# Optimization experiments

Measured on AMD Instinct MI355X. Metric: run time of the kernel, lower is better.

Reference implementation:

```python
import jax, jax.numpy as jnp
import numpy as np

K = 3          # per-row / per-col topk, from init kwarg k
THRESHOLD = 0.0


def setup_inputs() -> dict:
    key = jax.random.key(0)
    k1, k2 = jax.random.split(key)
    P, R, S = 512, 256, 256
    matching_score_map = jax.random.normal(k1, (P, R, S), dtype=jnp.float32)
    node_corr_scores = jax.random.uniform(k2, (P,), dtype=jnp.float32)
    ref_knn_masks = jnp.ones((P, R), dtype=bool)
    src_knn_masks = jnp.ones((P, S), dtype=bool)
    return {
        "matching_score_map": matching_score_map,
        "node_corr_scores": node_corr_scores,
        "ref_knn_masks": ref_knn_masks,
        "src_knn_masks": src_knn_masks,
    }


def reference(matching_score_map, node_corr_scores, ref_knn_masks, src_knn_masks):
    # score map: exp of log-matching scores  [P, R, S]
    score = jnp.exp(matching_score_map)
    P, R, S = score.shape
    # valid correspondence mask  [P, R, S]
    corr_mask = ref_knn_masks[:, :, None] & src_knn_masks[:, None, :]

    p_idx = jnp.arange(P)[:, None, None]

    # topk along src axis (dim=2), scatter back into a zero map
    ref_vals, ref_idx = jax.lax.top_k(score, K)                      # [P, R, K]
    ref_score_map = jnp.zeros_like(score).at[
        p_idx, jnp.arange(R)[None, :, None], ref_idx
    ].set(ref_vals)

    # topk along ref axis (dim=1): transpose so it is the last axis
    src_vals, src_idx = jax.lax.top_k(score.transpose(0, 2, 1), K)   # [P, S, K]
    src_score_map = jnp.zeros_like(score).at[
        p_idx, src_idx, jnp.arange(S)[None, :, None]
    ].set(src_vals)

    ref_corr_map = (ref_score_map > THRESHOLD) & corr_mask
    src_corr_map = (src_score_map > THRESHOLD) & corr_mask

    score_map = (ref_score_map + src_score_map) * 0.5
    # mutual=False -> logical_or; conditional=False -> no node_corr_scores scaling
    corr_map = ref_corr_map | src_corr_map
    return score_map, corr_map
```

## Files before the change

kernel.cpp:

```cpp
#include <hip/hip_runtime.h>
#include <math.h>
#include <stdint.h>

#define Pn 512
#define Rn 256
#define Sn 256

typedef unsigned long long u64;
typedef unsigned int u32;

__device__ __forceinline__ u32 mono(float f) {
  u32 u = __float_as_uint(f);
  return (u & 0x80000000u) ? ~u : (u | 0x80000000u);
}
__device__ __forceinline__ float unmono(u32 m) {
  u32 bits = (m & 0x80000000u) ? (m & 0x7FFFFFFFu) : ~m;
  return __uint_as_float(bits);
}
__device__ __forceinline__ u64 makekey(float v, int idx) {
  return ((u64)mono(v) << 32) | (u32)(~(u32)idx);
}
__device__ __forceinline__ int key_idx(u64 k) { return (int)(~(u32)k); }
__device__ __forceinline__ float key_val(u64 k) { return unmono((u32)(k >> 32)); }

__device__ __forceinline__ void cswap(u64& a, u64& b) {
  const bool c = a > b;
  const u64 hi = c ? a : b;
  const u64 lo = c ? b : a;
  a = hi; b = lo;
}

#define COL_BLOCKS Pn
#define ROW_BLOCKS ((Pn * Rn) / 4)

__global__ __launch_bounds__(256) void top3_kernel(
    const float* __restrict__ score,
    float* __restrict__ refv, int* __restrict__ refi,
    float* __restrict__ srcv, int* __restrict__ srci) {
  if (blockIdx.x < COL_BLOCKS) {
    const int p = blockIdx.x;
    const int s = threadIdx.x;
    const float* base = score + (size_t)p * Rn * Sn + s;
    u64 t0 = 0, t1 = 0, t2 = 0;
    #pragma unroll 8
    for (int r = 0; r < Rn; ++r) {
      u64 k = makekey(base[(size_t)r * Sn], r);
      cswap(t0, k); cswap(t1, k); cswap(t2, k);
    }
    const size_t PS = (size_t)Pn * Sn;
    const size_t o  = (size_t)p * Sn + s;
    srcv[0 * PS + o] = expf(key_val(t0)); srci[0 * PS + o] = key_idx(t0);
    srcv[1 * PS + o] = expf(key_val(t1)); srci[1 * PS + o] = key_idx(t1);
    srcv[2 * PS + o] = expf(key_val(t2)); srci[2 * PS + o] = key_idx(t2);
  } else {
    const int bid  = blockIdx.x - COL_BLOCKS;
    const int row  = (bid * blockDim.x + threadIdx.x) >> 6;
    const int lane = threadIdx.x & 63;
    const float4 v = reinterpret_cast<const float4*>(score + (size_t)row * Sn)[lane];
    const int b = lane * 4;
    u64 a0 = makekey(v.x, b + 0);
    u64 a1 = makekey(v.y, b + 1);
    u64 a2 = makekey(v.z, b + 2);
    u64 a3 = makekey(v.w, b + 3);
    cswap(a0, a1); cswap(a2, a3); cswap(a0, a2); cswap(a1, a3); cswap(a1, a2);
    u64 t0 = a0, t1 = a1, t2 = a2;

    u64 res0 = 0, res1 = 0, res2 = 0;
    #pragma unroll
    for (int j = 0; j < 3; ++j) {
      u64 m = t0;
      #pragma unroll
      for (int off = 1; off < 64; off <<= 1) {
        const u64 o = __shfl_xor(m, off);
        m = (o > m) ? o : m;
      }
      const bool hit = (t0 == m);
      t0 = hit ? t1 : t0;
      t1 = hit ? t2 : t1;
      t2 = hit ? 0ull : t2;
      if (j == 0) res0 = m; else if (j == 1) res1 = m; else res2 = m;
    }
    if (lane == 0) {
      const size_t o = (size_t)row * 3;
      refv[o + 0] = expf(key_val(res0)); refi[o + 0] = key_idx(res0);
      refv[o + 1] = expf(key_val(res1)); refi[o + 1] = key_idx(res1);
      refv[o + 2] = expf(key_val(res2)); refi[o + 2] = key_idx(res2);
    }
  }
}

__device__ __forceinline__ void compute_elem(
    int s, int r, bool rmask, int sm,
    float rv0, float rv1, float rv2, int ri0, int ri1, int ri2,
    float a0, int b0, float a1, int b1, float a2, int b2,
    float& oscore, float& ocorr) {
  const float rv = (s == ri0) ? rv0 : (s == ri1) ? rv1 : (s == ri2) ? rv2 : 0.0f;
  const float sv = (r == b0) ? a0 : (r == b1) ? a1 : (r == b2) ? a2 : 0.0f;
  oscore = 0.5f * (rv + sv);
  const bool m = rmask && (sm != 0);
  ocorr = (((rv > 0.0f) || (sv > 0.0f)) && m) ? 1.0f : 0.0f;
}

__global__ __launch_bounds__(256) void write_kernel(
    const float* __restrict__ refv, const int* __restrict__ refi,
    const float* __restrict__ srcv, const int* __restrict__ srci,
    const int* __restrict__ rmaskp, const int* __restrict__ smaskp,
    float* __restrict__ out) {
  const int p     = blockIdx.x >> 2;
  const int rbase = (blockIdx.x & 3) * 64;
  const int warp  = threadIdx.x >> 6;
  const int lane  = threadIdx.x & 63;
  const size_t PS = (size_t)Pn * Sn;
  const size_t N  = (size_t)Pn * Rn * Sn;

  const float4 sv0 = reinterpret_cast<const float4*>(srcv + 0 * PS + (size_t)p * Sn)[lane];
  const float4 sv1 = reinterpret_cast<const float4*>(srcv + 1 * PS + (size_t)p * Sn)[lane];
  const float4 sv2 = reinterpret_cast<const float4*>(srcv + 2 * PS + (size_t)p * Sn)[lane];
  const int4   si0 = reinterpret_cast<const int4*>(srci + 0 * PS + (size_t)p * Sn)[lane];
  const int4   si1 = reinterpret_cast<const int4*>(srci + 1 * PS + (size_t)p * Sn)[lane];
  const int4   si2 = reinterpret_cast<const int4*>(srci + 2 * PS + (size_t)p * Sn)[lane];
  const int4   sm  = reinterpret_cast<const int4*>(smaskp + (size_t)p * Sn)[lane];
  const int sbase = lane * 4;

  #pragma unroll 4
  for (int it = 0; it < 16; ++it) {
    const int r   = rbase + it * 4 + warp;
    const int row = p * Rn + r;
    const size_t rb = (size_t)row * 3;
    const float rv0 = refv[rb + 0], rv1 = refv[rb + 1], rv2 = refv[rb + 2];
    const int   ri0 = refi[rb + 0], ri1 = refi[rb + 1], ri2 = refi[rb + 2];
    const bool  rmask = rmaskp[row] != 0;

    float4 osc, oco;
    compute_elem(sbase + 0, r, rmask, sm.x, rv0, rv1, rv2, ri0, ri1, ri2,
                 sv0.x, si0.x, sv1.x, si1.x, sv2.x, si2.x, osc.x, oco.x);
    compute_elem(sbase + 1, r, rmask, sm.y, rv0, rv1, rv2, ri0, ri1, ri2,
                 sv0.y, si0.y, sv1.y, si1.y, sv2.y, si2.y, osc.y, oco.y);
    compute_elem(sbase + 2, r, rmask, sm.z, rv0, rv1, rv2, ri0, ri1, ri2,
                 sv0.z, si0.z, sv1.z, si1.z, sv2.z, si2.z, osc.z, oco.z);
    compute_elem(sbase + 3, r, rmask, sm.w, rv0, rv1, rv2, ri0, ri1, ri2,
                 sv0.w, si0.w, sv1.w, si1.w, sv2.w, si2.w, osc.w, oco.w);

    reinterpret_cast<float4*>(out + (size_t)row * Sn)[lane]     = osc;
    reinterpret_cast<float4*>(out + N + (size_t)row * Sn)[lane] = oco;
  }
}

extern "C" void kernel_launch(void* const* d_in, const int* in_sizes, int n_in,
                              void* d_out, int out_size, void* d_ws, size_t ws_size,
                              hipStream_t stream) {
  const float* score = (const float*)d_in[0];
  const int* rmask = (const int*)d_in[2];
  const int* smask = (const int*)d_in[3];
  float* out = (float*)d_out;

  const size_t PR = (size_t)Pn * Rn;
  const size_t PS = (size_t)Pn * Sn;
  float* refv = (float*)d_ws;
  int*   refi = (int*)(refv + 3 * PR);
  float* srcv = (float*)(refi + 3 * PR);
  int*   srci = (int*)(srcv + 3 * PS);

  top3_kernel<<<COL_BLOCKS + ROW_BLOCKS, 256, 0, stream>>>(score, refv, refi, srcv, srci);
  write_kernel<<<(Pn * Rn) / 64, 256, 0, stream>>>(refv, refi, srcv, srci,
                                                   rmask, smask, out);
}
```

Baseline: 436.2 us.

## Split column top-3 into four row slabs and merge partials in write kernel

The column-wise top-3 pass previously used one block per P, with each thread serially scanning all 256 rows. That long dependent loop across only 512 blocks likely formed the critical path. It is now split into four slabs of 64 rows, giving four times as many blocks, and each slab writes its partial top-3 to workspace. The write kernel merges the 12 partial candidates per column and applies exp there. The insertion also compares plain floats instead of packed 64-bit keys. The cost is extra workspace traffic and redundant merges across the four blocks that share each p. Tie-breaking order may also differ slightly from before.

```diff
diff --git a/kernel.cpp b/kernel.cpp
--- a/kernel.cpp
+++ b/kernel.cpp
@@ -22,7 +22,6 @@
 }
 __device__ __forceinline__ int key_idx(u64 k) { return (int)(~(u32)k); }
 __device__ __forceinline__ float key_val(u64 k) { return unmono((u32)(k >> 32)); }
-
 __device__ __forceinline__ void cswap(u64& a, u64& b) {
   const bool c = a > b;
   const u64 hi = c ? a : b;
@@ -30,30 +29,43 @@
   a = hi; b = lo;
 }
 
-#define COL_BLOCKS Pn
+__device__ __forceinline__ void ins3f(float v, int i,
+    float& t0, int& i0, float& t1, int& i1, float& t2, int& i2) {
+  const bool b0 = v > t0, b1 = v > t1, b2 = v > t2;
+  const float nt0 = b0 ? v : t0;
+  const int   ni0 = b0 ? i : i0;
+  const float nt1 = b0 ? t0 : (b1 ? v : t1);
+  const int   ni1 = b0 ? i0 : (b1 ? i : i1);
+  const float nt2 = b1 ? t1 : (b2 ? v : t2);
+  const int   ni2 = b1 ? i1 : (b2 ? i : i2);
+  t0 = nt0; i0 = ni0; t1 = nt1; i1 = ni1; t2 = nt2; i2 = ni2;
+}
+
+#define COLSLAB_BLOCKS (Pn * 4)
 #define ROW_BLOCKS ((Pn * Rn) / 4)
 
 __global__ __launch_bounds__(256) void top3_kernel(
     const float* __restrict__ score,
     float* __restrict__ refv, int* __restrict__ refi,
-    float* __restrict__ srcv, int* __restrict__ srci) {
-  if (blockIdx.x < COL_BLOCKS) {
-    const int p = blockIdx.x;
-    const int s = threadIdx.x;
-    const float* base = score + (size_t)p * Rn * Sn + s;
-    u64 t0 = 0, t1 = 0, t2 = 0;
+    float* __restrict__ colpv, int* __restrict__ colpi) {
+  const size_t PS = (size_t)Pn * Sn;
+  if (blockIdx.x < COLSLAB_BLOCKS) {
+    const int p    = blockIdx.x >> 2;
+    const int slab = blockIdx.x & 3;
+    const int s    = threadIdx.x;
+    const float* base = score + (size_t)p * Rn * Sn + (size_t)slab * 64 * Sn + s;
+    float t0 = -INFINITY, t1 = -INFINITY, t2 = -INFINITY;
+    int   i0 = -1, i1 = -1, i2 = -1;
+    const int r0 = slab * 64;
     #pragma unroll 8
-    for (int r = 0; r < Rn; ++r) {
-      u64 k = makekey(base[(size_t)r * Sn], r);
-      cswap(t0, k); cswap(t1, k); cswap(t2, k);
-    }
-    const size_t PS = (size_t)Pn * Sn;
-    const size_t o  = (size_t)p * Sn + s;
-    srcv[0 * PS + o] = expf(key_val(t0)); srci[0 * PS + o] = key_idx(t0);
-    srcv[1 * PS + o] = expf(key_val(t1)); srci[1 * PS + o] = key_idx(t1);
-    srcv[2 * PS + o] = expf(key_val(t2)); srci[2 * PS + o] = key_idx(t2);
+    for (int r = 0; r < 64; ++r)
+      ins3f(base[(size_t)r * Sn], r0 + r, t0, i0, t1, i1, t2, i2);
+    const size_t o = (size_t)p * Sn + s;
+    colpv[(slab * 3 + 0) * PS + o] = t0; colpi[(slab * 3 + 0) * PS + o] = i0;
+    colpv[(slab * 3 + 1) * PS + o] = t1; colpi[(slab * 3 + 1) * PS + o] = i1;
+    colpv[(slab * 3 + 2) * PS + o] = t2; colpi[(slab * 3 + 2) * PS + o] = i2;
   } else {
-    const int bid  = blockIdx.x - COL_BLOCKS;
+    const int bid  = blockIdx.x - COLSLAB_BLOCKS;
     const int row  = (bid * blockDim.x + threadIdx.x) >> 6;
     const int lane = threadIdx.x & 63;
     const float4 v = reinterpret_cast<const float4*>(score + (size_t)row * Sn)[lane];
@@ -103,7 +115,7 @@
 
 __global__ __launch_bounds__(256) void write_kernel(
     const float* __restrict__ refv, const int* __restrict__ refi,
-    const float* __restrict__ srcv, const int* __restrict__ srci,
+    const float* __restrict__ colpv, const int* __restrict__ colpi,
     const int* __restrict__ rmaskp, const int* __restrict__ smaskp,
     float* __restrict__ out) {
   const int p     = blockIdx.x >> 2;
@@ -112,15 +124,30 @@
   const int lane  = threadIdx.x & 63;
   const size_t PS = (size_t)Pn * Sn;
   const size_t N  = (size_t)Pn * Rn * Sn;
+  const size_t cb = (size_t)p * Sn;
 
-  const float4 sv0 = reinterpret_cast<const float4*>(srcv + 0 * PS + (size_t)p * Sn)[lane];
-  const float4 sv1 = reinterpret_cast<const float4*>(srcv + 1 * PS + (size_t)p * Sn)[lane];
-  const float4 sv2 = reinterpret_cast<const float4*>(srcv + 2 * PS + (size_t)p * Sn)[lane];
-  const int4   si0 = reinterpret_cast<const int4*>(srci + 0 * PS + (size_t)p * Sn)[lane];
-  const int4   si1 = reinterpret_cast<const int4*>(srci + 1 * PS + (size_t)p * Sn)[lane];
-  const int4   si2 = reinterpret_cast<const int4*>(srci + 2 * PS + (size_t)p * Sn)[lane];
-  const int4   sm  = reinterpret_cast<const int4*>(smaskp + (size_t)p * Sn)[lane];
+  float4 T0 = reinterpret_cast<const float4*>(colpv + 0 * PS + cb)[lane];
+  float4 T1 = reinterpret_cast<const float4*>(colpv + 1 * PS + cb)[lane];
+  float4 T2 = reinterpret_cast<const float4*>(colpv + 2 * PS + cb)[lane];
+  int4   I0 = reinterpret_cast<const int4*>(colpi + 0 * PS + cb)[lane];
+  int4   I1 = reinterpret_cast<const int4*>(colpi + 1 * PS + cb)[lane];
+  int4   I2 = reinterpret_cast<const int4*>(colpi + 2 * PS + cb)[lane];
+  #pragma unroll
+  for (int sk = 3; sk < 12; ++sk) {
+    const float4 V = reinterpret_cast<const float4*>(colpv + (size_t)sk * PS + cb)[lane];
+    const int4   I = reinterpret_cast<const int4*>(colpi + (size_t)sk * PS + cb)[lane];
+    ins3f(V.x, I.x, T0.x, I0.x, T1.x, I1.x, T2.x, I2.x);
+    ins3f(V.y, I.y, T0.y, I0.y, T1.y, I1.y, T2.y, I2.y);
+    ins3f(V.z, I.z, T0.z, I0.z, T1.z, I1.z, T2.z, I2.z);
+    ins3f(V.w, I.w, T0.w, I0.w, T1.w, I1.w, T2.w, I2.w);
+  }
+  T0.x = expf(T0.x); T0.y = expf(T0.y); T0.z = expf(T0.z); T0.w = expf(T0.w);
+  T1.x = expf(T1.x); T1.y = expf(T1.y); T1.z = expf(T1.z); T1.w = expf(T1.w);
+  T2.x = expf(T2.x); T2.y = expf(T2.y); T2.z = expf(T2.z); T2.w = expf(T2.w);
+
+  const int4 sm = reinterpret_cast<const int4*>(smaskp + cb)[lane];
   const int sbase = lane * 4;
+  float* outp = out + (size_t)p * Rn * Sn;
 
   #pragma unroll 4
   for (int it = 0; it < 16; ++it) {
@@ -129,20 +156,20 @@
     const size_t rb = (size_t)row * 3;
     const float rv0 = refv[rb + 0], rv1 = refv[rb + 1], rv2 = refv[rb + 2];
     const int   ri0 = refi[rb + 0], ri1 = refi[rb + 1], ri2 = refi[rb + 2];
-    const bool  rmask = rmaskp[row] != 0;
+    const bool  rm  = rmaskp[row] != 0;
 
     float4 osc, oco;
-    compute_elem(sbase + 0, r, rmask, sm.x, rv0, rv1, rv2, ri0, ri1, ri2,
-                 sv0.x, si0.x, sv1.x, si1.x, sv2.x, si2.x, osc.x, oco.x);
-    compute_elem(sbase + 1, r, rmask, sm.y, rv0, rv1, rv2, ri0, ri1, ri2,
-                 sv0.y, si0.y, sv1.y, si1.y, sv2.y, si2.y, osc.y, oco.y);
-    compute_elem(sbase + 2, r, rmask, sm.z, rv0, rv1, rv2, ri0, ri1, ri2,
-                 sv0.z, si0.z, sv1.z, si1.z, sv2.z, si2.z, osc.z, oco.z);
-    compute_elem(sbase + 3, r, rmask, sm.w, rv0, rv1, rv2, ri0, ri1, ri2,
-                 sv0.w, si0.w, sv1.w, si1.w, sv2.w, si2.w, osc.w, oco.w);
+    compute_elem(sbase + 0, r, rm, sm.x, rv0, rv1, rv2, ri0, ri1, ri2,
+                 T0.x, I0.x, T1.x, I1.x, T2.x, I2.x, osc.x, oco.x);
+    compute_elem(sbase + 1, r, rm, sm.y, rv0, rv1, rv2, ri0, ri1, ri2,
+                 T0.y, I0.y, T1.y, I1.y, T2.y, I2.y, osc.y, oco.y);
+    compute_elem(sbase + 2, r, rm, sm.z, rv0, rv1, rv2, ri0, ri1, ri2,
+                 T0.z, I0.z, T1.z, I1.z, T2.z, I2.z, osc.z, oco.z);
+    compute_elem(sbase + 3, r, rm, sm.w, rv0, rv1, rv2, ri0, ri1, ri2,
+                 T0.w, I0.w, T1.w, I1.w, T2.w, I2.w, osc.w, oco.w);
 
-    reinterpret_cast<float4*>(out + (size_t)row * Sn)[lane]     = osc;
-    reinterpret_cast<float4*>(out + N + (size_t)row * Sn)[lane] = oco;
+    reinterpret_cast<float4*>(outp + (size_t)r * Sn)[lane]     = osc;
+    reinterpret_cast<float4*>(outp + N + (size_t)r * Sn)[lane] = oco;
   }
 }
 
@@ -156,12 +183,13 @@
 
   const size_t PR = (size_t)Pn * Rn;
   const size_t PS = (size_t)Pn * Sn;
-  float* refv = (float*)d_ws;
-  int*   refi = (int*)(refv + 3 * PR);
-  float* srcv = (float*)(refi + 3 * PR);
-  int*   srci = (int*)(srcv + 3 * PS);
+  float* refv  = (float*)d_ws;
+  int*   refi  = (int*)(refv + 3 * PR);
+  float* colpv = (float*)(refi + 3 * PR);
+  int*   colpi = (int*)(colpv + 12 * PS);
 
-  top3_kernel<<<COL_BLOCKS + ROW_BLOCKS, 256, 0, stream>>>(score, refv, refi, srcv, srci);
-  write_kernel<<<(Pn * Rn) / 64, 256, 0, stream>>>(refv, refi, srcv, srci,
-                                                   rmask, smask, out);
+  top3_kernel<<<COLSLAB_BLOCKS + ROW_BLOCKS, 256, 0, stream>>>(
+      score, refv, refi, colpv, colpi);
+  write_kernel<<<(Pn * Rn) / 64, 256, 0, stream>>>(
+      refv, refi, colpv, colpi, rmask, smask, out);
 }
```

Result: slower. 466.2 us (+6.9%).
